# Performance work log

Hardware: AMD Instinct MI355X
Metric: run time of the kernel (lower is better)

Reference implementation:

```python
import jax, jax.numpy as jnp
import numpy as np

B, F, H, W = 1, 6, 20, 26
S = F * H * W            # 3120 tokens
DIM, NH, HD = 1536, 12, 128
C = HD // 2              # 64 rotary channels
T_C = C - 2 * (C // 3)   # 22 temporal channels
H_C = C // 3             # 21
W_C = C // 3             # 21
LOCAL_FRAMES = 4         # local_attn_size (in frames)
SINK_FRAMES = 1          # sink_size (in frames)
EPS = 1e-6
MAX_POS = 1024


def _angle_table(n_ch):
    inv = 1.0 / (10000.0 ** (np.arange(n_ch, dtype=np.float64) / n_ch))
    return np.outer(np.arange(MAX_POS, dtype=np.float64), inv)


def setup_inputs() -> dict:
    key = jax.random.key(0)
    ks = jax.random.split(key, 8)
    sc = 0.02
    ang = np.concatenate([_angle_table(T_C), _angle_table(H_C), _angle_table(W_C)], axis=1)  # [1024, 64]
    return {
        "x": jax.random.normal(ks[0], (B, S, DIM), jnp.float32),
        "seq_lens": jnp.array([S], jnp.int32),
        "grid_sizes": jnp.array([[F, H, W]], jnp.int32),
        "freqs_cos": jnp.asarray(np.cos(ang), jnp.float32),
        "freqs_sin": jnp.asarray(np.sin(ang), jnp.float32),
        "Wq": jax.random.normal(ks[1], (DIM, DIM), jnp.float32) * sc,
        "bq": jnp.zeros((DIM,), jnp.float32),
        "Wk": jax.random.normal(ks[2], (DIM, DIM), jnp.float32) * sc,
        "bk": jnp.zeros((DIM,), jnp.float32),
        "Wv": jax.random.normal(ks[3], (DIM, DIM), jnp.float32) * sc,
        "bv": jnp.zeros((DIM,), jnp.float32),
        "Wo": jax.random.normal(ks[4], (DIM, DIM), jnp.float32) * sc,
        "bo": jnp.zeros((DIM,), jnp.float32),
        "gq": jnp.ones((DIM,), jnp.float32),
        "gk": jnp.ones((DIM,), jnp.float32),
    }


def _rms_norm(x, g):
    # WanRMSNorm: x * rsqrt(mean(x^2) + eps) * weight
    return x * jax.lax.rsqrt(jnp.mean(x * x, axis=-1, keepdims=True) + EPS) * g


def _rope_apply(x, freqs_cos, freqs_sin):
    # x: [B, S, NH, HD]; per-token 3D (f,h,w) rotary on consecutive pairs.
    pos = jnp.arange(S)
    f = pos // (H * W)
    hh = (pos // W) % H
    ww = pos % W
    cos_t, cos_h, cos_w = freqs_cos[:, :T_C], freqs_cos[:, T_C:T_C + H_C], freqs_cos[:, T_C + H_C:]
    sin_t, sin_h, sin_w = freqs_sin[:, :T_C], freqs_sin[:, T_C:T_C + H_C], freqs_sin[:, T_C + H_C:]
    cos = jnp.concatenate([cos_t[f], cos_h[hh], cos_w[ww]], axis=-1)[None, :, None, :]  # [1,S,1,C]
    sin = jnp.concatenate([sin_t[f], sin_h[hh], sin_w[ww]], axis=-1)[None, :, None, :]
    xp = x.reshape(B, S, NH, C, 2)
    xr, xi = xp[..., 0], xp[..., 1]
    out = jnp.stack([xr * cos - xi * sin, xr * sin + xi * cos], axis=-1)
    return out.reshape(B, S, NH, HD)


def _block_mask():
    # frame-causal + local window (in frames) + sink frames: [S, S] bool
    fid = jnp.arange(S) // (H * W)
    fi, fj = fid[:, None], fid[None, :]
    return (fj <= fi) & ((fi - fj < LOCAL_FRAMES) | (fj < SINK_FRAMES))


def reference(x, seq_lens, grid_sizes, freqs_cos, freqs_sin,
              Wq, bq, Wk, bk, Wv, bv, Wo, bo, gq, gk):
    q = _rms_norm(x @ Wq + bq, gq).reshape(B, S, NH, HD)
    k = _rms_norm(x @ Wk + bk, gk).reshape(B, S, NH, HD)
    v = (x @ Wv + bv).reshape(B, S, NH, HD)
    rq = _rope_apply(q, freqs_cos, freqs_sin)
    rk = _rope_apply(k, freqs_cos, freqs_sin)
    scale = 1.0 / jnp.sqrt(jnp.asarray(HD, x.dtype))
    scores = jnp.einsum('bind,bjnd->bnij', rq, rk) * scale  # [B,NH,S,S]
    scores = jnp.where(_block_mask()[None, None], scores, jnp.finfo(scores.dtype).min)
    attn = jax.nn.softmax(scores, axis=-1)
    out = jnp.einsum('bnij,bjnd->bind', attn, v).reshape(B, S, DIM)
    return out @ Wo + bo
```

## Files before the change

kernel.cpp:

```cpp
#include <hip/hip_runtime.h>
#include <hip/hip_bf16.h>
#include <stdint.h>

typedef short v8s __attribute__((ext_vector_type(8)));
typedef float v4f __attribute__((ext_vector_type(4)));
typedef unsigned short u16;

#define S_LEN 3120
#define DIMN 1536
#define NHEAD 12
#define HDIM 128
#define FRM 520
#define NT64 49
#define T64_PH 166
#define TOT64 1992
#define SCALE_QK 0.088388347648318447f
#define MAXOFF 12.0f
#define LOG2E 1.4426950408889634f
#define SC2 (SCALE_QK * LOG2E)

__device__ __forceinline__ v4f mfma16(v8s a, v8s b, v4f c) {
  return __builtin_amdgcn_mfma_f32_16x16x32_bf16(a, b, c, 0, 0, 0);
}
__device__ __forceinline__ float b2f(u16 u) {
  union { float f; unsigned int i; } x; x.i = ((unsigned int)u) << 16; return x.f;
}
__device__ __forceinline__ u16 f2b(float f) {
  union { float f; unsigned int i; } x; x.f = f;
  unsigned int r = x.i + 0x7FFFu + ((x.i >> 16) & 1u);
  return (u16)(r >> 16);
}
__device__ __forceinline__ void async16(const void* g, void* l) {
  __builtin_amdgcn_global_load_lds(
      (__attribute__((address_space(1))) const void*)g,
      (__attribute__((address_space(3))) void*)l, 16, 0, 0);
}

__global__ void detect_dtype(const u16* __restrict__ w, int* __restrict__ flag) {
  __shared__ int sh;
  int t = threadIdx.x;
  if (t == 0) sh = 0;
  __syncthreads();
  u16 m0 = (u16)(w[2 * t] & 0x7FFF);
  u16 m1 = (u16)(w[2 * t + 1] & 0x7FFF);
  if (m0 >= 0x4480 || m1 >= 0x4480) atomicOr(&sh, 1);
  __syncthreads();
  if (t == 0) *flag = sh;
}

struct PrepArgs {
  const void* tin[4]; u16* tout[4];
  const void* csrc[9]; u16* cdst[9]; int cn[9];
};
__global__ __launch_bounds__(256) void prep(PrepArgs a, const int* __restrict__ flag) {
  int isf = *flag;
  int z = blockIdx.z;
  int t = threadIdx.x;
  if (z < 4) {
    __shared__ u16 tile[32][33];
    const float* inf = (const float*)a.tin[z];
    const u16* inb = (const u16*)a.tin[z];
    u16* out = a.tout[z];
    int tx = t & 31, ty = t >> 5;
    int gr0 = blockIdx.y * 32, gc0 = blockIdx.x * 32;
#pragma unroll
    for (int i = 0; i < 4; ++i) {
      int r = ty + i * 8;
      size_t idx = (size_t)(gr0 + r) * DIMN + gc0 + tx;
      tile[r][tx] = isf ? f2b(inf[idx]) : inb[idx];
    }
    __syncthreads();
#pragma unroll
    for (int i = 0; i < 4; ++i) {
      int r = ty + i * 8;
      out[(size_t)(gc0 + r) * DIMN + gr0 + tx] = tile[tx][r];
    }
  } else {
    int id = z - 4;
    int n = a.cn[id];
    const float* sf = (const float*)a.csrc[id];
    const u16* sb = (const u16*)a.csrc[id];
    u16* d = a.cdst[id];
    int bidx = blockIdx.y * gridDim.x + blockIdx.x;
    int stride = gridDim.x * gridDim.y * 256;
    for (int i = bidx * 256 + t; i < n; i += stride)
      d[i] = isf ? f2b(sf[i]) : sb[i];
  }
}

__global__ __launch_bounds__(256) void transpose16(const u16* __restrict__ in,
                                                   u16* __restrict__ out,
                                                   int rows, int cols) {
  __shared__ u16 tile[32][33];
  int t = threadIdx.x;
  int tx = t & 31, ty = t >> 5;
  int gr0 = blockIdx.y * 32, gc0 = blockIdx.x * 32;
#pragma unroll
  for (int i = 0; i < 4; ++i) {
    int r = ty + i * 8;
    int gr = gr0 + r, gc = gc0 + tx;
    if (gr < rows && gc < cols) tile[r][tx] = in[(size_t)gr * cols + gc];
  }
  __syncthreads();
#pragma unroll
  for (int i = 0; i < 4; ++i) {
    int r = ty + i * 8;
    int orow = gc0 + r, ocol = gr0 + tx;
    if (orow < cols && ocol < rows) out[(size_t)orow * rows + ocol] = tile[tx][r];
  }
}

template <int MT>
__global__ __launch_bounds__(256) void gemm3(
    const u16* __restrict__ A,
    const u16* BT0, const u16* BT1, const u16* BT2,
    const u16* b0, const u16* b1, const u16* b2,
    void* C0, void* C1, void* C2, int M, const int* __restrict__ flag, int dyn) {
  const u16* BT; const u16* bias; void* C;
  if (blockIdx.z == 0)      { BT = BT0; bias = b0; C = C0; }
  else if (blockIdx.z == 1) { BT = BT1; bias = b1; C = C1; }
  else                      { BT = BT2; bias = b2; C = C2; }
  int f32out = dyn ? *flag : 0;
  __shared__ __align__(16) short As[MT * 64];
  __shared__ __align__(16) short Bs[128 * 64];
  int t = threadIdx.x, w = t >> 6, l = t & 63;
  int ln = l & 15, lg = l >> 4;
  int m0 = blockIdx.y * MT, n0 = blockIdx.x * 128;
  int lr = l >> 3;
  int gl = (l & 7) ^ lr;
  constexpr int ACH = MT / 32;
  const u16* gAp[ACH]; short* lAp[ACH];
#pragma unroll
  for (int i = 0; i < ACH; ++i) {
    int c = w * ACH + i;
    int arow = min(m0 + c * 8 + lr, M - 1);
    gAp[i] = A + (size_t)arow * DIMN + gl * 8;
    lAp[i] = As + c * 512;
  }
  const u16* gBp[4]; short* lBp[4];
#pragma unroll
  for (int i = 0; i < 4; ++i) {
    int c = w * 4 + i;
    int brow = n0 + c * 8 + lr;
    gBp[i] = BT + (size_t)brow * DIMN + gl * 8;
    lBp[i] = Bs + c * 512;
  }
  constexpr int NJ = (MT == 128) ? 4 : 2;
  int wm = (MT == 128) ? (w & 1) : 0;
  int wn = (MT == 128) ? (w >> 1) : w;
  int aoff[2][4], boff[2][NJ];
#pragma unroll
  for (int ks = 0; ks < 2; ++ks) {
#pragma unroll
    for (int i = 0; i < 4; ++i) {
      int ar = wm * 64 + i * 16 + ln;
      aoff[ks][i] = ar * 64 + (((ks * 4 + lg) ^ (ar & 7)) * 8);
    }
#pragma unroll
    for (int j = 0; j < NJ; ++j) {
      int br = wn * (NJ * 16) + j * 16 + ln;
      boff[ks][j] = br * 64 + (((ks * 4 + lg) ^ (br & 7)) * 8);
    }
  }
  v4f acc[4][NJ] = {};
  for (int k0 = 0; k0 < DIMN; k0 += 64) {
    __syncthreads();
#pragma unroll
    for (int i = 0; i < ACH; ++i) async16(gAp[i] + k0, lAp[i]);
#pragma unroll
    for (int i = 0; i < 4; ++i) async16(gBp[i] + k0, lBp[i]);
    __syncthreads();
#pragma unroll
    for (int ks = 0; ks < 2; ++ks) {
      v8s af[4], bfr[NJ];
#pragma unroll
      for (int i = 0; i < 4; ++i) af[i] = *(const v8s*)(As + aoff[ks][i]);
#pragma unroll
      for (int j = 0; j < NJ; ++j) bfr[j] = *(const v8s*)(Bs + boff[ks][j]);
#pragma unroll
      for (int i = 0; i < 4; ++i)
#pragma unroll
        for (int j = 0; j < NJ; ++j) acc[i][j] = mfma16(af[i], bfr[j], acc[i][j]);
    }
  }
#pragma unroll
  for (int i = 0; i < 4; ++i) {
    int rb = m0 + wm * 64 + i * 16 + lg * 4;
#pragma unroll
    for (int j = 0; j < NJ; ++j) {
      int col = n0 + wn * (NJ * 16) + j * 16 + ln;
      float bv = b2f(bias[col]);
#pragma unroll
      for (int r = 0; r < 4; ++r) {
        int grow = rb + r;
        if (grow < M) {
          size_t idx = (size_t)grow * DIMN + col;
          float val = acc[i][j][r] + bv;
          if (f32out) ((float*)C)[idx] = val;
          else        ((u16*)C)[idx] = f2b(val);
        }
      }
    }
  }
}

__global__ __launch_bounds__(256) void norm_rope(u16* __restrict__ Q, u16* __restrict__ K,
                                                 const u16* __restrict__ gq,
                                                 const u16* __restrict__ gk,
                                                 const u16* __restrict__ fcos,
                                                 const u16* __restrict__ fsin) {
  int s = blockIdx.x;
  u16* base = (blockIdx.y == 0 ? Q : K) + (size_t)s * DIMN;
  const u16* g = (blockIdx.y == 0) ? gq : gk;
  int t = threadIdx.x;
  int e = t * 6;
  float x[6];
#pragma unroll
  for (int i = 0; i < 6; ++i) x[i] = b2f(base[e + i]);
  float ss = 0.f;
#pragma unroll
  for (int i = 0; i < 6; ++i) ss += x[i] * x[i];
#pragma unroll
  for (int off = 32; off > 0; off >>= 1) ss += __shfl_xor(ss, off);
  __shared__ float red[4];
  if ((t & 63) == 0) red[t >> 6] = ss;
  __syncthreads();
  float tot = red[0] + red[1] + red[2] + red[3];
  float rs = rsqrtf(tot * (1.0f / DIMN) + 1e-6f);
  int f = s / FRM;
  int hh = (s / 26) % 20;
  int ww = s % 26;
#pragma unroll
  for (int u = 0; u < 3; ++u) {
    int e0 = e + 2 * u;
    int c = (e0 & 127) >> 1;
    int p = (c < 22) ? f : ((c < 43) ? hh : ww);
    float co = b2f(fcos[p * 64 + c]);
    float si = b2f(fsin[p * 64 + c]);
    float xr = x[2 * u] * rs * b2f(g[e0]);
    float xi = x[2 * u + 1] * rs * b2f(g[e0 + 1]);
    base[e0]     = f2b(xr * co - xi * si);
    base[e0 + 1] = f2b(xr * si + xi * co);
  }
}

__global__ __launch_bounds__(128) void attn_block(const u16* __restrict__ Q,
                                                  const u16* __restrict__ K,
                                                  const u16* __restrict__ VT,
                                                  u16* __restrict__ Po,
                                                  float* __restrict__ Pl) {
  __shared__ __align__(16) short Ks[32 * 128];
  __shared__ __align__(16) short Pt[2][32 * 40];
  int t = threadIdx.x, w = t >> 6, l = t & 63;
  int ln = l & 15, lg = l >> 4;
  int task = blockIdx.x;
  int head = task / T64_PH, tid = task % T64_PH;
  int tile = 0, frame = 0;
  {
    int acc = 0;
    for (tile = 0; tile < NT64; ++tile) {
      int q0t = tile * 64;
      int f_lo = q0t / FRM;
      int f_hi = min(q0t + 63, S_LEN - 1) / FRM;
      int fstart = max(0, f_lo - 3);
      int sink = fstart > 0;
      int nf = f_hi - fstart + 1 + sink;
      if (tid < acc + nf) {
        int c = tid - acc;
        frame = sink ? (c == 0 ? 0 : fstart + c - 1) : (fstart + c);
        break;
      }
      acc += nf;
    }
  }
  int q0 = tile * 64 + w * 32;
  v8s qf[2][4];
  float bias[2][4];
  bool rowok[2][4];
#pragma unroll
  for (int g = 0; g < 2; ++g) {
    int row = min(q0 + g * 16 + ln, S_LEN - 1);
    const u16* qp = Q + (size_t)row * DIMN + head * HDIM + lg * 8;
#pragma unroll
    for (int c = 0; c < 4; ++c) qf[g][c] = *(const v8s*)(qp + c * 32);
#pragma unroll
    for (int r = 0; r < 4; ++r) {
      int qr = q0 + g * 16 + lg * 4 + r;
      int fi = (qr < S_LEN) ? qr / FRM : -1;
      rowok[g][r] = (frame <= fi) && ((fi - frame) < 4 || frame == 0);
      bias[g][r] = rowok[g][r] ? (-MAXOFF * LOG2E) : -1.0e4f;
    }
  }
  float lsum[2][4] = {};
  v4f o[2][8] = {};
  int kbeg = frame * FRM;
  const u16* kp[4]; char* kd[4];
#pragma unroll
  for (int i = 0; i < 4; ++i) {
    int n = (w * 4 + i) * 64 + l;
    int kr = n >> 4;
    int kgl = (n & 15) ^ (kr & 15);
    kp[i] = K + (size_t)(kbeg + kr) * DIMN + head * HDIM + kgl * 8;
    kd[i] = (char*)Ks + (size_t)(w * 4 + i) * 1024;
  }
  const u16* vp[8];
#pragma unroll
  for (int d = 0; d < 8; ++d)
    vp[d] = VT + (size_t)(head * HDIM + d * 16 + ln) * S_LEN + kbeg + lg * 8;

#define ATTN_STEP(KB, PEEL)                                                      \
  {                                                                              \
    __syncthreads();                                                             \
    _Pragma("unroll") for (int i = 0; i < 4; ++i) async16(kp[i], kd[i]);         \
    v8s vf[8];                                                                   \
    _Pragma("unroll") for (int d = 0; d < 8; ++d) vf[d] = *(const v8s*)vp[d];    \
    __syncthreads();                                                             \
    v4f s[2][2] = {};                                                            \
    _Pragma("unroll") for (int kg = 0; kg < 2; ++kg) {                           \
      _Pragma("unroll") for (int c = 0; c < 4; ++c) {                            \
        v8s kf = *(const v8s*)(&Ks[(kg * 16 + ln) * 128 + (((c * 4 + lg) ^ ln) * 8)]); \
        s[0][kg] = mfma16(qf[0][c], kf, s[0][kg]);                               \
        s[1][kg] = mfma16(qf[1][c], kf, s[1][kg]);                               \
      }                                                                          \
    }                                                                            \
    _Pragma("unroll") for (int g = 0; g < 2; ++g)                                \
      _Pragma("unroll") for (int kg = 0; kg < 2; ++kg) {                         \
        bool jv = !PEEL || ((KB) + kg * 16 + ln) < kbeg + FRM;                   \
        _Pragma("unroll") for (int r = 0; r < 4; ++r) {                          \
          float p = __builtin_amdgcn_exp2f(fmaf(s[g][kg][r], SC2, bias[g][r]));  \
          if (PEEL && !jv) p = 0.f;                                              \
          unsigned int bi = __float_as_uint(p) & 0xffff0000u;                    \
          lsum[g][r] += __uint_as_float(bi);                                     \
          Pt[w][(g * 16 + lg * 4 + r) * 40 + kg * 16 + ln] = (u16)(bi >> 16);    \
        }                                                                        \
      }                                                                          \
    v8s pf0 = *(const v8s*)(&Pt[w][ln * 40 + lg * 8]);                           \
    v8s pf1 = *(const v8s*)(&Pt[w][(16 + ln) * 40 + lg * 8]);                    \
    _Pragma("unroll") for (int d = 0; d < 8; ++d) {                              \
      o[0][d] = mfma16(pf0, vf[d], o[0][d]);                                     \
      o[1][d] = mfma16(pf1, vf[d], o[1][d]);                                     \
    }                                                                            \
    _Pragma("unroll") for (int i = 0; i < 4; ++i) kp[i] += 32 * DIMN;            \
    _Pragma("unroll") for (int d = 0; d < 8; ++d) vp[d] += 32;                   \
  }

  for (int it = 0; it < 16; ++it) ATTN_STEP(kbeg + it * 32, 0);
  ATTN_STEP(kbeg + 512, 1);
#undef ATTN_STEP

#pragma unroll
  for (int g = 0; g < 2; ++g)
#pragma unroll
    for (int r = 0; r < 4; ++r) {
      float v = lsum[g][r];
      v += __shfl_xor(v, 1);
      v += __shfl_xor(v, 2);
      v += __shfl_xor(v, 4);
      v += __shfl_xor(v, 8);
      lsum[g][r] = v;
    }
  size_t pbase = (size_t)task * (64 * 128);
#pragma unroll
  for (int g = 0; g < 2; ++g)
#pragma unroll
    for (int d = 0; d < 8; ++d)
#pragma unroll
      for (int r = 0; r < 4; ++r) {
        int lrow = w * 32 + g * 16 + lg * 4 + r;
        Po[pbase + lrow * 128 + d * 16 + ln] = f2b(o[g][d][r]);
      }
  if (ln == 0) {
#pragma unroll
    for (int g = 0; g < 2; ++g)
#pragma unroll
      for (int r = 0; r < 4; ++r)
        Pl[task * 64 + w * 32 + g * 16 + lg * 4 + r] = lsum[g][r];
  }
}

__global__ __launch_bounds__(256) void attn_combine(const u16* __restrict__ Po,
                                                    const float* __restrict__ Pl,
                                                    u16* __restrict__ Oa) {
  int tile = blockIdx.x, h = blockIdx.y;
  int accv = 0, nf = 0;
  for (int q = 0; q < NT64; ++q) {
    int q0t = q * 64;
    int f_lo = q0t / FRM;
    int f_hi = min(q0t + 63, S_LEN - 1) / FRM;
    int fstart = max(0, f_lo - 3);
    int sink = fstart > 0;
    nf = f_hi - fstart + 1 + sink;
    if (q == tile) break;
    accv += nf;
  }
  int base = h * T64_PH + accv;
  int t = threadIdx.x;
  int row = t >> 2, seg = (t & 3) * 32;
  int grow = tile * 64 + row;
  if (grow >= S_LEN) return;
  float lsum = 0.f;
  float ao[32];
#pragma unroll
  for (int j = 0; j < 32; ++j) ao[j] = 0.f;
  for (int c = 0; c < nf; ++c) {
    int task = base + c;
    lsum += Pl[task * 64 + row];
    const u16* p = Po + (size_t)task * 8192 + row * 128 + seg;
#pragma unroll
    for (int v = 0; v < 4; ++v) {
      v8s x = *(const v8s*)(p + v * 8);
#pragma unroll
      for (int j = 0; j < 8; ++j) ao[v * 8 + j] += b2f((u16)x[j]);
    }
  }
  float inv = 1.0f / lsum;
  u16* dst = Oa + (size_t)grow * DIMN + h * HDIM + seg;
#pragma unroll
  for (int v = 0; v < 4; ++v) {
    v8s res;
#pragma unroll
    for (int j = 0; j < 8; ++j) res[j] = (short)f2b(ao[v * 8 + j] * inv);
    *(v8s*)(dst + v * 8) = res;
  }
}

extern "C" void kernel_launch(void* const* d_in, const int* in_sizes, int n_in,
                              void* d_out, int out_size, void* d_ws, size_t ws_size,
                              hipStream_t stream) {
  (void)n_in; (void)out_size; (void)ws_size;
  int* flag = (int*)d_ws;
  u16* ws = (u16*)d_ws;
  size_t off = 16;
  const size_t SD = (size_t)S_LEN * DIMN;
  const size_t WW = (size_t)DIMN * DIMN;
  const size_t NPO = (size_t)1032 * 128 * 128;
  auto alloc = [&](size_t n) { u16* p = ws + off; off += (n + 7) & ~(size_t)7; return p; };
  u16* Xc  = alloc(SD + 64);
  u16* Fc  = alloc(65536);
  u16* Fs  = alloc(65536);
  u16* bqc = alloc(1536); u16* bkc = alloc(1536); u16* bvc = alloc(1536); u16* boc = alloc(1536);
  u16* gqc = alloc(1536); u16* gkc = alloc(1536);
  u16* Qr = alloc(SD); u16* Kr = alloc(SD + 64 * DIMN);
  u16* Vr = alloc(SD); u16* Oa = alloc(SD);
  u16* WoT = alloc(WW);
  u16* WqT = alloc(WW); u16* WkT = alloc(WW); u16* WvT = alloc(WW);
  alloc(NPO - 3 * WW);
  float* Pl = (float*)alloc((size_t)TOT64 * 64 * 2);
  u16* Po = WqT;
  u16* VT = Xc;

  detect_dtype<<<1, 256, 0, stream>>>((const u16*)d_in[5], flag);

  PrepArgs pa;
  pa.tin[0] = d_in[5];  pa.tout[0] = WqT;
  pa.tin[1] = d_in[7];  pa.tout[1] = WkT;
  pa.tin[2] = d_in[9];  pa.tout[2] = WvT;
  pa.tin[3] = d_in[11]; pa.tout[3] = WoT;
  const int srcIdx[9] = {0, 3, 4, 6, 8, 10, 12, 13, 14};
  u16* dsts[9] = {Xc, Fc, Fs, bqc, bkc, bvc, boc, gqc, gkc};
  for (int i = 0; i < 9; ++i) {
    pa.csrc[i] = d_in[srcIdx[i]];
    pa.cdst[i] = dsts[i];
    pa.cn[i] = in_sizes[srcIdx[i]];
  }
  dim3 b256(256);
  prep<<<dim3(48, 48, 13), b256, 0, stream>>>(pa, flag);
  gemm3<64><<<dim3(12, 49, 3), b256, 0, stream>>>(Xc, WqT, WkT, WvT, bqc, bkc, bvc,
                                                  Qr, Kr, Vr, S_LEN, flag, 0);
  norm_rope<<<dim3(S_LEN, 2), b256, 0, stream>>>(Qr, Kr, gqc, gkc, Fc, Fs);
  transpose16<<<dim3(48, 98), b256, 0, stream>>>(Vr, VT, S_LEN, DIMN);
  attn_block<<<dim3(TOT64), dim3(128), 0, stream>>>(Qr, Kr, VT, Po, Pl);
  attn_combine<<<dim3(NT64, NHEAD), b256, 0, stream>>>(Po, Pl, Oa);
  gemm3<64><<<dim3(12, 49, 1), b256, 0, stream>>>(Oa, WoT, WoT, WoT, boc, boc, boc,
                                                  d_out, d_out, d_out, S_LEN, flag, 1);
}
```

Before: 375.5 us.

## Double-buffer K tiles in LDS with async prefetch of the next tile

The attention kernel now holds two LDS buffers for K. It issues the async global-to-LDS copy of the next 32-row K tile before computing on the current one, and drops one of the two barriers per step. The goal is to hide K load latency behind the QK and PV MFMA work instead of stalling on each tile. In exchange, K shared memory per block doubles, which may lower occupancy, and correctness relies on the top-of-step barrier also waiting for the outstanding async copies.

```diff
diff --git a/kernel.cpp b/kernel.cpp
--- a/kernel.cpp
+++ b/kernel.cpp
@@ -249,7 +249,7 @@
                                                   const u16* __restrict__ VT,
                                                   u16* __restrict__ Po,
                                                   float* __restrict__ Pl) {
-  __shared__ __align__(16) short Ks[32 * 128];
+  __shared__ __align__(16) short Ks[2][32 * 128];
   __shared__ __align__(16) short Pt[2][32 * 40];
   int t = threadIdx.x, w = t >> 6, l = t & 63;
   int ln = l & 15, lg = l >> 4;
@@ -276,7 +276,6 @@
   int q0 = tile * 64 + w * 32;
   v8s qf[2][4];
   float bias[2][4];
-  bool rowok[2][4];
 #pragma unroll
   for (int g = 0; g < 2; ++g) {
     int row = min(q0 + g * 16 + ln, S_LEN - 1);
@@ -287,45 +286,56 @@
     for (int r = 0; r < 4; ++r) {
       int qr = q0 + g * 16 + lg * 4 + r;
       int fi = (qr < S_LEN) ? qr / FRM : -1;
-      rowok[g][r] = (frame <= fi) && ((fi - frame) < 4 || frame == 0);
-      bias[g][r] = rowok[g][r] ? (-MAXOFF * LOG2E) : -1.0e4f;
+      bool ok = (frame <= fi) && ((fi - frame) < 4 || frame == 0);
+      bias[g][r] = ok ? (-MAXOFF * LOG2E) : -1.0e4f;
     }
   }
   float lsum[2][4] = {};
   v4f o[2][8] = {};
   int kbeg = frame * FRM;
-  const u16* kp[4]; char* kd[4];
+  const u16* kp[4]; int kdo[4];
 #pragma unroll
   for (int i = 0; i < 4; ++i) {
     int n = (w * 4 + i) * 64 + l;
     int kr = n >> 4;
     int kgl = (n & 15) ^ (kr & 15);
     kp[i] = K + (size_t)(kbeg + kr) * DIMN + head * HDIM + kgl * 8;
-    kd[i] = (char*)Ks + (size_t)(w * 4 + i) * 1024;
+    kdo[i] = (w * 4 + i) * 1024;
   }
   const u16* vp[8];
 #pragma unroll
   for (int d = 0; d < 8; ++d)
     vp[d] = VT + (size_t)(head * HDIM + d * 16 + ln) * S_LEN + kbeg + lg * 8;
 
-#define ATTN_STEP(KB, PEEL)                                                      \
+#pragma unroll
+  for (int i = 0; i < 4; ++i) {
+    async16(kp[i], (char*)(&Ks[0][0]) + kdo[i]);
+    kp[i] += 32 * DIMN;
+  }
+
+#define ATTN_STEP(IT, PEEL)                                                      \
   {                                                                              \
-    __syncthreads();                                                             \
-    _Pragma("unroll") for (int i = 0; i < 4; ++i) async16(kp[i], kd[i]);         \
+    const int cur = (IT) & 1;                                                    \
+    __syncthreads();       \
     v8s vf[8];                                                                   \
-    _Pragma("unroll") for (int d = 0; d < 8; ++d) vf[d] = *(const v8s*)vp[d];    \
-    __syncthreads();                                                             \
+    _Pragma("unroll") for (int d = 0; d < 8; ++d) { vf[d] = *(const v8s*)vp[d]; vp[d] += 32; } \
+    if (!PEEL) {       \
+      _Pragma("unroll") for (int i = 0; i < 4; ++i) {                            \
+        async16(kp[i], (char*)(&Ks[cur ^ 1][0]) + kdo[i]);                       \
+        kp[i] += 32 * DIMN;                                                      \
+      }                                                                          \
+    }                                                                            \
     v4f s[2][2] = {};                                                            \
     _Pragma("unroll") for (int kg = 0; kg < 2; ++kg) {                           \
       _Pragma("unroll") for (int c = 0; c < 4; ++c) {                            \
-        v8s kf = *(const v8s*)(&Ks[(kg * 16 + ln) * 128 + (((c * 4 + lg) ^ ln) * 8)]); \
+        v8s kf = *(const v8s*)(&Ks[cur][(kg * 16 + ln) * 128 + (((c * 4 + lg) ^ ln) * 8)]); \
         s[0][kg] = mfma16(qf[0][c], kf, s[0][kg]);                               \
         s[1][kg] = mfma16(qf[1][c], kf, s[1][kg]);                               \
       }                                                                          \
     }                                                                            \
     _Pragma("unroll") for (int g = 0; g < 2; ++g)                                \
       _Pragma("unroll") for (int kg = 0; kg < 2; ++kg) {                         \
-        bool jv = !PEEL || ((KB) + kg * 16 + ln) < kbeg + FRM;                   \
+        bool jv = !PEEL || (kbeg + 512 + kg * 16 + ln) < kbeg + FRM;             \
         _Pragma("unroll") for (int r = 0; r < 4; ++r) {                          \
           float p = __builtin_amdgcn_exp2f(fmaf(s[g][kg][r], SC2, bias[g][r]));  \
           if (PEEL && !jv) p = 0.f;                                              \
@@ -340,12 +350,10 @@
       o[0][d] = mfma16(pf0, vf[d], o[0][d]);                                     \
       o[1][d] = mfma16(pf1, vf[d], o[1][d]);                                     \
     }                                                                            \
-    _Pragma("unroll") for (int i = 0; i < 4; ++i) kp[i] += 32 * DIMN;            \
-    _Pragma("unroll") for (int d = 0; d < 8; ++d) vp[d] += 32;                   \
-  }
-
-  for (int it = 0; it < 16; ++it) ATTN_STEP(kbeg + it * 32, 0);
-  ATTN_STEP(kbeg + 512, 1);
+  }
+
+  for (int it = 0; it < 16; ++it) ATTN_STEP(it, 0);
+  ATTN_STEP(16, 1);
 #undef ATTN_STEP
 
 #pragma unroll
```

New measurement: 375.6 us. No clear change (+0.0%).

## Fuse V transpose into QKV GEMM epilogue and merge split-frame attention blocks

Applied to the files above, without the earlier changes.

The QKV GEMM now writes V directly in transposed layout from its epilogue, which removes the separate transpose kernel. Attention is restructured from one block per (query tile, key frame) with partial outputs and a combine kernel into one block per (query tile, head). Each block loops over its 4-6 key frames and normalizes in registers, which eliminates the Po/Pl round-trip and the combine launch. The cost is far fewer blocks (588 instead of 1992) with longer serial work each, which risks load imbalance and lower occupancy. Tiles are issued in reverse order to schedule the heavy ones first. The transposed V stores are strided 4-element writes that may coalesce poorly.

```diff
diff --git a/kernel.cpp b/kernel.cpp
--- a/kernel.cpp
+++ b/kernel.cpp
@@ -3,6 +3,7 @@
 #include <stdint.h>
 
 typedef short v8s __attribute__((ext_vector_type(8)));
+typedef short v4s __attribute__((ext_vector_type(4)));
 typedef float v4f __attribute__((ext_vector_type(4)));
 typedef unsigned short u16;
 
@@ -12,8 +13,7 @@
 #define HDIM 128
 #define FRM 520
 #define NT64 49
-#define T64_PH 166
-#define TOT64 1992
+#define NBLK 588
 #define SCALE_QK 0.088388347648318447f
 #define MAXOFF 12.0f
 #define LOG2E 1.4426950408889634f
@@ -88,34 +88,13 @@
   }
 }
 
-__global__ __launch_bounds__(256) void transpose16(const u16* __restrict__ in,
-                                                   u16* __restrict__ out,
-                                                   int rows, int cols) {
-  __shared__ u16 tile[32][33];
-  int t = threadIdx.x;
-  int tx = t & 31, ty = t >> 5;
-  int gr0 = blockIdx.y * 32, gc0 = blockIdx.x * 32;
-#pragma unroll
-  for (int i = 0; i < 4; ++i) {
-    int r = ty + i * 8;
-    int gr = gr0 + r, gc = gc0 + tx;
-    if (gr < rows && gc < cols) tile[r][tx] = in[(size_t)gr * cols + gc];
-  }
-  __syncthreads();
-#pragma unroll
-  for (int i = 0; i < 4; ++i) {
-    int r = ty + i * 8;
-    int orow = gc0 + r, ocol = gr0 + tx;
-    if (orow < cols && ocol < rows) out[(size_t)orow * rows + ocol] = tile[tx][r];
-  }
-}
-
 template <int MT>
 __global__ __launch_bounds__(256) void gemm3(
     const u16* __restrict__ A,
     const u16* BT0, const u16* BT1, const u16* BT2,
     const u16* b0, const u16* b1, const u16* b2,
-    void* C0, void* C1, void* C2, int M, const int* __restrict__ flag, int dyn) {
+    void* C0, void* C1, void* C2, int M, const int* __restrict__ flag, int dyn,
+    int vtz) {
   const u16* BT; const u16* bias; void* C;
   if (blockIdx.z == 0)      { BT = BT0; bias = b0; C = C0; }
   else if (blockIdx.z == 1) { BT = BT1; bias = b1; C = C1; }
@@ -183,6 +162,28 @@
         for (int j = 0; j < NJ; ++j) acc[i][j] = mfma16(af[i], bfr[j], acc[i][j]);
     }
   }
+  if ((int)blockIdx.z == vtz) {
+#pragma unroll
+    for (int i = 0; i < 4; ++i) {
+      int rb = m0 + wm * 64 + i * 16 + lg * 4;
+#pragma unroll
+      for (int j = 0; j < NJ; ++j) {
+        int col = n0 + wn * (NJ * 16) + j * 16 + ln;
+        float bv = b2f(bias[col]);
+        v4s tmp;
+#pragma unroll
+        for (int r = 0; r < 4; ++r) tmp[r] = (short)f2b(acc[i][j][r] + bv);
+        u16* dst = (u16*)C + (size_t)col * S_LEN + rb;
+        if (rb + 3 < M) {
+          *(v4s*)dst = tmp;
+        } else {
+#pragma unroll
+          for (int r = 0; r < 4; ++r) if (rb + r < M) dst[r] = (u16)tmp[r];
+        }
+      }
+    }
+    return;
+  }
 #pragma unroll
   for (int i = 0; i < 4; ++i) {
     int rb = m0 + wm * 64 + i * 16 + lg * 4;
@@ -247,36 +248,25 @@
 __global__ __launch_bounds__(128) void attn_block(const u16* __restrict__ Q,
                                                   const u16* __restrict__ K,
                                                   const u16* __restrict__ VT,
-                                                  u16* __restrict__ Po,
-                                                  float* __restrict__ Pl) {
+                                                  u16* __restrict__ Oa) {
   __shared__ __align__(16) short Ks[32 * 128];
   __shared__ __align__(16) short Pt[2][32 * 40];
   int t = threadIdx.x, w = t >> 6, l = t & 63;
   int ln = l & 15, lg = l >> 4;
   int task = blockIdx.x;
-  int head = task / T64_PH, tid = task % T64_PH;
-  int tile = 0, frame = 0;
-  {
-    int acc = 0;
-    for (tile = 0; tile < NT64; ++tile) {
-      int q0t = tile * 64;
-      int f_lo = q0t / FRM;
-      int f_hi = min(q0t + 63, S_LEN - 1) / FRM;
-      int fstart = max(0, f_lo - 3);
-      int sink = fstart > 0;
-      int nf = f_hi - fstart + 1 + sink;
-      if (tid < acc + nf) {
-        int c = tid - acc;
-        frame = sink ? (c == 0 ? 0 : fstart + c - 1) : (fstart + c);
-        break;
-      }
-      acc += nf;
-    }
-  }
-  int q0 = tile * 64 + w * 32;
+  int head = task % NHEAD;
+  int tile = NT64 - 1 - (task / NHEAD);
+  int q0t = tile * 64;
+  int f_lo = q0t / FRM;
+  int f_hi = min(q0t + 63, S_LEN - 1) / FRM;
+  int fstart = max(0, f_lo - 3);
+  int frames[6]; int nf = 0;
+  if (fstart > 0) frames[nf++] = 0;
+  for (int f = fstart; f <= f_hi; ++f) frames[nf++] = f;
+
+  int q0 = q0t + w * 32;
   v8s qf[2][4];
-  float bias[2][4];
-  bool rowok[2][4];
+  int fi[2][4];
 #pragma unroll
   for (int g = 0; g < 2; ++g) {
     int row = min(q0 + g * 16 + ln, S_LEN - 1);
@@ -286,34 +276,48 @@
 #pragma unroll
     for (int r = 0; r < 4; ++r) {
       int qr = q0 + g * 16 + lg * 4 + r;
-      int fi = (qr < S_LEN) ? qr / FRM : -1;
-      rowok[g][r] = (frame <= fi) && ((fi - frame) < 4 || frame == 0);
-      bias[g][r] = rowok[g][r] ? (-MAXOFF * LOG2E) : -1.0e4f;
+      fi[g][r] = (qr < S_LEN) ? qr / FRM : -1;
     }
   }
   float lsum[2][4] = {};
   v4f o[2][8] = {};
-  int kbeg = frame * FRM;
-  const u16* kp[4]; char* kd[4];
+  int kr_i[4], kgl_i[4], kdo_i[4];
 #pragma unroll
   for (int i = 0; i < 4; ++i) {
     int n = (w * 4 + i) * 64 + l;
-    int kr = n >> 4;
-    int kgl = (n & 15) ^ (kr & 15);
-    kp[i] = K + (size_t)(kbeg + kr) * DIMN + head * HDIM + kgl * 8;
-    kd[i] = (char*)Ks + (size_t)(w * 4 + i) * 1024;
-  }
-  const u16* vp[8];
-#pragma unroll
-  for (int d = 0; d < 8; ++d)
-    vp[d] = VT + (size_t)(head * HDIM + d * 16 + ln) * S_LEN + kbeg + lg * 8;
-
-#define ATTN_STEP(KB, PEEL)                                                      \
+    kr_i[i] = n >> 4;
+    kgl_i[i] = (n & 15) ^ (kr_i[i] & 15);
+    kdo_i[i] = (w * 4 + i) * 1024;
+  }
+
+  for (int u = 0; u < nf; ++u) {
+    int frame = frames[u];
+    int kbeg = frame * FRM;
+    float bias[2][4];
+#pragma unroll
+    for (int g = 0; g < 2; ++g)
+#pragma unroll
+      for (int r = 0; r < 4; ++r) {
+        bool ok = (frame <= fi[g][r]) && ((fi[g][r] - frame) < 4 || frame == 0);
+        bias[g][r] = ok ? (-MAXOFF * LOG2E) : -1.0e4f;
+      }
+    const u16* kp[4]; const u16* vp[8];
+#pragma unroll
+    for (int i = 0; i < 4; ++i)
+      kp[i] = K + (size_t)(kbeg + kr_i[i]) * DIMN + head * HDIM + kgl_i[i] * 8;
+#pragma unroll
+    for (int d = 0; d < 8; ++d)
+      vp[d] = VT + (size_t)(head * HDIM + d * 16 + ln) * S_LEN + kbeg + lg * 8;
+
+#define ATTN_STEP(PEEL)                                                          \
   {                                                                              \
     __syncthreads();                                                             \
-    _Pragma("unroll") for (int i = 0; i < 4; ++i) async16(kp[i], kd[i]);         \
+    _Pragma("unroll") for (int i = 0; i < 4; ++i) {                              \
+      async16(kp[i], (char*)Ks + kdo_i[i]);                                      \
+      kp[i] += 32 * DIMN;                                                        \
+    }                                                                            \
     v8s vf[8];                                                                   \
-    _Pragma("unroll") for (int d = 0; d < 8; ++d) vf[d] = *(const v8s*)vp[d];    \
+    _Pragma("unroll") for (int d = 0; d < 8; ++d) { vf[d] = *(const v8s*)vp[d]; vp[d] += 32; } \
     __syncthreads();                                                             \
     v4f s[2][2] = {};                                                            \
     _Pragma("unroll") for (int kg = 0; kg < 2; ++kg) {                           \
@@ -325,7 +329,7 @@
     }                                                                            \
     _Pragma("unroll") for (int g = 0; g < 2; ++g)                                \
       _Pragma("unroll") for (int kg = 0; kg < 2; ++kg) {                         \
-        bool jv = !PEEL || ((KB) + kg * 16 + ln) < kbeg + FRM;                   \
+        bool jv = !PEEL || (512 + kg * 16 + ln) < FRM;                           \
         _Pragma("unroll") for (int r = 0; r < 4; ++r) {                          \
           float p = __builtin_amdgcn_exp2f(fmaf(s[g][kg][r], SC2, bias[g][r]));  \
           if (PEEL && !jv) p = 0.f;                                              \
@@ -340,14 +344,14 @@
       o[0][d] = mfma16(pf0, vf[d], o[0][d]);                                     \
       o[1][d] = mfma16(pf1, vf[d], o[1][d]);                                     \
     }                                                                            \
-    _Pragma("unroll") for (int i = 0; i < 4; ++i) kp[i] += 32 * DIMN;            \
-    _Pragma("unroll") for (int d = 0; d < 8; ++d) vp[d] += 32;                   \
-  }
-
-  for (int it = 0; it < 16; ++it) ATTN_STEP(kbeg + it * 32, 0);
-  ATTN_STEP(kbeg + 512, 1);
+  }
+
+    for (int it = 0; it < 16; ++it) ATTN_STEP(0);
+    ATTN_STEP(1);
 #undef ATTN_STEP
-
+  }
+
+  float inv[2][4];
 #pragma unroll
   for (int g = 0; g < 2; ++g)
 #pragma unroll
@@ -357,71 +361,20 @@
       v += __shfl_xor(v, 2);
       v += __shfl_xor(v, 4);
       v += __shfl_xor(v, 8);
-      lsum[g][r] = v;
-    }
-  size_t pbase = (size_t)task * (64 * 128);
+      inv[g][r] = 1.0f / v;
+    }
 #pragma unroll
   for (int g = 0; g < 2; ++g)
 #pragma unroll
-    for (int d = 0; d < 8; ++d)
-#pragma unroll
-      for (int r = 0; r < 4; ++r) {
-        int lrow = w * 32 + g * 16 + lg * 4 + r;
-        Po[pbase + lrow * 128 + d * 16 + ln] = f2b(o[g][d][r]);
+    for (int r = 0; r < 4; ++r) {
+      int grow = q0 + g * 16 + lg * 4 + r;
+      if (grow < S_LEN) {
+        u16* dst = Oa + (size_t)grow * DIMN + head * HDIM + ln;
+#pragma unroll
+        for (int d = 0; d < 8; ++d)
+          dst[d * 16] = f2b(o[g][d][r] * inv[g][r]);
       }
-  if (ln == 0) {
-#pragma unroll
-    for (int g = 0; g < 2; ++g)
-#pragma unroll
-      for (int r = 0; r < 4; ++r)
-        Pl[task * 64 + w * 32 + g * 16 + lg * 4 + r] = lsum[g][r];
-  }
-}
-
-__global__ __launch_bounds__(256) void attn_combine(const u16* __restrict__ Po,
-                                                    const float* __restrict__ Pl,
-                                                    u16* __restrict__ Oa) {
-  int tile = blockIdx.x, h = blockIdx.y;
-  int accv = 0, nf = 0;
-  for (int q = 0; q < NT64; ++q) {
-    int q0t = q * 64;
-    int f_lo = q0t / FRM;
-    int f_hi = min(q0t + 63, S_LEN - 1) / FRM;
-    int fstart = max(0, f_lo - 3);
-    int sink = fstart > 0;
-    nf = f_hi - fstart + 1 + sink;
-    if (q == tile) break;
-    accv += nf;
-  }
-  int base = h * T64_PH + accv;
-  int t = threadIdx.x;
-  int row = t >> 2, seg = (t & 3) * 32;
-  int grow = tile * 64 + row;
-  if (grow >= S_LEN) return;
-  float lsum = 0.f;
-  float ao[32];
-#pragma unroll
-  for (int j = 0; j < 32; ++j) ao[j] = 0.f;
-  for (int c = 0; c < nf; ++c) {
-    int task = base + c;
-    lsum += Pl[task * 64 + row];
-    const u16* p = Po + (size_t)task * 8192 + row * 128 + seg;
-#pragma unroll
-    for (int v = 0; v < 4; ++v) {
-      v8s x = *(const v8s*)(p + v * 8);
-#pragma unroll
-      for (int j = 0; j < 8; ++j) ao[v * 8 + j] += b2f((u16)x[j]);
-    }
-  }
-  float inv = 1.0f / lsum;
-  u16* dst = Oa + (size_t)grow * DIMN + h * HDIM + seg;
-#pragma unroll
-  for (int v = 0; v < 4; ++v) {
-    v8s res;
-#pragma unroll
-    for (int j = 0; j < 8; ++j) res[j] = (short)f2b(ao[v * 8 + j] * inv);
-    *(v8s*)(dst + v * 8) = res;
-  }
+    }
 }
 
 extern "C" void kernel_launch(void* const* d_in, const int* in_sizes, int n_in,
@@ -433,21 +386,18 @@
   size_t off = 16;
   const size_t SD = (size_t)S_LEN * DIMN;
   const size_t WW = (size_t)DIMN * DIMN;
-  const size_t NPO = (size_t)1032 * 128 * 128;
   auto alloc = [&](size_t n) { u16* p = ws + off; off += (n + 7) & ~(size_t)7; return p; };
-  u16* Xc  = alloc(SD + 64);
+  u16* Xc  = alloc(SD);
   u16* Fc  = alloc(65536);
   u16* Fs  = alloc(65536);
   u16* bqc = alloc(1536); u16* bkc = alloc(1536); u16* bvc = alloc(1536); u16* boc = alloc(1536);
   u16* gqc = alloc(1536); u16* gkc = alloc(1536);
-  u16* Qr = alloc(SD); u16* Kr = alloc(SD + 64 * DIMN);
-  u16* Vr = alloc(SD); u16* Oa = alloc(SD);
+  u16* Qr = alloc(SD);
+  u16* Kr = alloc(SD + (size_t)64 * DIMN);
+  u16* VT = alloc(SD + 128);
+  u16* Oa = alloc(SD);
   u16* WoT = alloc(WW);
   u16* WqT = alloc(WW); u16* WkT = alloc(WW); u16* WvT = alloc(WW);
-  alloc(NPO - 3 * WW);
-  float* Pl = (float*)alloc((size_t)TOT64 * 64 * 2);
-  u16* Po = WqT;
-  u16* VT = Xc;
 
   detect_dtype<<<1, 256, 0, stream>>>((const u16*)d_in[5], flag);
 
@@ -466,11 +416,9 @@
   dim3 b256(256);
   prep<<<dim3(48, 48, 13), b256, 0, stream>>>(pa, flag);
   gemm3<64><<<dim3(12, 49, 3), b256, 0, stream>>>(Xc, WqT, WkT, WvT, bqc, bkc, bvc,
-                                                  Qr, Kr, Vr, S_LEN, flag, 0);
+                                                  Qr, Kr, VT, S_LEN, flag, 0, 2);
   norm_rope<<<dim3(S_LEN, 2), b256, 0, stream>>>(Qr, Kr, gqc, gkc, Fc, Fs);
-  transpose16<<<dim3(48, 98), b256, 0, stream>>>(Vr, VT, S_LEN, DIMN);
-  attn_block<<<dim3(TOT64), dim3(128), 0, stream>>>(Qr, Kr, VT, Po, Pl);
-  attn_combine<<<dim3(NT64, NHEAD), b256, 0, stream>>>(Po, Pl, Oa);
+  attn_block<<<dim3(NBLK), dim3(128), 0, stream>>>(Qr, Kr, VT, Oa);
   gemm3<64><<<dim3(12, 49, 1), b256, 0, stream>>>(Oa, WoT, WoT, WoT, boc, boc, boc,
-                                                  d_out, d_out, d_out, S_LEN, flag, 1);
-}
+                                                  d_out, d_out, d_out, S_LEN, flag, 1, -1);
+}
```

Result: slower. 400.8 us (+6.7%).
